# Kernel tuning notes

Measured on AMD Instinct MI355X. Metric: run time of the kernel, lower is better.

## Reference

```python
import jax, jax.numpy as jnp
import numpy as np
from jax import lax

K = 3      # kernel_size
PAD = 1    # padding
OG = 2     # offset groups


def _conv2d(x, w, b):
    y = lax.conv_general_dilated(x, w, (1, 1), [(PAD, PAD), (PAD, PAD)],
                                 dimension_numbers=('NCHW', 'OIHW', 'NCHW'))
    return y + b[None, :, None, None]


def _deform_conv2d(x, offset, mask, weight):
    # torchvision-style modulated deform_conv2d (v2), stride=1, dilation=1,
    # zero out-of-bounds, offset layout [B, OG*K*K*2, H, W] with (dy, dx) pairs.
    B, C, H, W = x.shape
    O = weight.shape[0]
    K2 = K * K
    Cg = C // OG

    ki, kj = jnp.meshgrid(jnp.arange(K), jnp.arange(K), indexing='ij')
    ki = ki.reshape(K2)
    kj = kj.reshape(K2)
    base_y = jnp.arange(H)[None, :] - PAD + ki[:, None]   # [K2, H]
    base_x = jnp.arange(W)[None, :] - PAD + kj[:, None]   # [K2, W]

    off = offset.reshape(B, OG, K2, 2, H, W)
    py = off[:, :, :, 0] + base_y[None, None, :, :, None].astype(x.dtype)  # [B,OG,K2,H,W]
    px = off[:, :, :, 1] + base_x[None, None, :, None, :].astype(x.dtype)
    m = mask.reshape(B, OG, K2, H, W)

    y0f = jnp.floor(py)
    x0f = jnp.floor(px)
    wy1 = py - y0f   # bilinear weights, grads flow through py/px
    wx1 = px - x0f
    y0 = y0f.astype(jnp.int32)
    x0 = x0f.astype(jnp.int32)
    y1 = y0 + 1
    x1 = x0 + 1

    img = x.reshape(B, OG, Cg, H * W)

    def gather(yi, xi):
        valid = (yi >= 0) & (yi < H) & (xi >= 0) & (xi < W)
        idx = jnp.clip(yi, 0, H - 1) * W + jnp.clip(xi, 0, W - 1)          # [B,OG,K2,H,W]
        v = jnp.take_along_axis(img[:, :, :, None, :],
                                idx.reshape(B, OG, 1, K2, H * W), axis=-1)
        return v.reshape(B, OG, Cg, K2, H, W) * valid[:, :, None].astype(x.dtype)

    v00 = gather(y0, x0)
    v01 = gather(y0, x1)
    v10 = gather(y1, x0)
    v11 = gather(y1, x1)

    wy1e = wy1[:, :, None]   # [B,OG,1,K2,H,W]
    wx1e = wx1[:, :, None]
    val = (v00 * (1 - wy1e) * (1 - wx1e)
           + v01 * (1 - wy1e) * wx1e
           + v10 * wy1e * (1 - wx1e)
           + v11 * wy1e * wx1e)
    val = val * m[:, :, None]                               # modulation mask

    wr = weight.reshape(O, OG, Cg, K2)
    return jnp.einsum('ogck,bgckhw->bohw', wr, val)


def setup_inputs() -> dict:
    key = jax.random.key(0)
    k1, k2, k3, k4, k5 = jax.random.split(key, 5)
    B, C, O, H, W = 4, 64, 64, 128, 128
    K2 = K * K
    x = jax.random.normal(k1, (B, C, H, W), dtype=jnp.float32)
    w_main = jax.random.normal(k2, (O, C, K, K), dtype=jnp.float32) / np.sqrt(C * K2)
    w_off = jax.random.normal(k3, (2 * OG * K2, C, K, K), dtype=jnp.float32) * 0.01
    b_off = jax.random.normal(k4, (2 * OG * K2,), dtype=jnp.float32) * 0.01
    w_mask = jnp.full((OG * K2, C, K, K), 0.5, dtype=jnp.float32)  # init_mask = 0.5
    b_mask = jax.random.normal(k5, (OG * K2,), dtype=jnp.float32) * 0.01
    return {"x": x, "w_main": w_main, "w_off": w_off, "b_off": b_off,
            "w_mask": w_mask, "b_mask": b_mask}


def reference(x, w_main, w_off, b_off, w_mask, b_mask):
    offset = _conv2d(x, w_off, b_off)
    mask = jax.nn.sigmoid(_conv2d(x, w_mask, b_mask))
    return _deform_conv2d(x, offset, mask, w_main)
```

## Files before the change

kernel.cpp:

```cpp
#include <hip/hip_runtime.h>
#include <math.h>

#define BB 4
#define C 64
#define O 64
#define H 128
#define W 128
#define OG 2
#define Cg 32
#define K2 9
#define HW (H*W)
#define NOFF 36
#define NMSK 18

typedef __bf16 bf16;
typedef bf16 bf16x8 __attribute__((ext_vector_type(8)));
typedef float f32x4 __attribute__((ext_vector_type(4)));
typedef unsigned short u16x4 __attribute__((ext_vector_type(4)));

#define VSTR 288
#define BSTR 60

__device__ inline unsigned short f2h_bits(float f) {
  _Float16 h = (_Float16)f;
  return __builtin_bit_cast(unsigned short, h);
}
__device__ inline float h2f(unsigned short u) {
  return (float)__builtin_bit_cast(_Float16, u);
}

__global__ __launch_bounds__(256) void transpose_nhwc(
    const float* __restrict__ x, unsigned short* __restrict__ xT) {
  __shared__ float tile[64][65];
  int tid = threadIdx.x;
  int b = blockIdx.x >> 8;
  int p0 = (blockIdx.x & 255) * 64;
#pragma unroll
  for (int it = 0; it < 16; ++it) {
    int c = it * 4 + (tid >> 6);
    tile[c][tid & 63] = x[((size_t)(b * C + c)) * HW + p0 + (tid & 63)];
  }
  __syncthreads();
#pragma unroll
  for (int it = 0; it < 4; ++it) {
    int p = it * 16 + (tid >> 4);
    int cg = tid & 15;
    u16x4 o;
#pragma unroll
    for (int j = 0; j < 4; ++j) {
      bf16 t = (bf16)tile[cg * 4 + j][p];
      o[j] = __builtin_bit_cast(unsigned short, t);
    }
    *(u16x4*)&xT[((size_t)(b * HW + p0 + p)) * C + cg * 4] = o;
  }
}

__global__ __launch_bounds__(256) void prep_w(
    const float* __restrict__ w_main, const float* __restrict__ w_off,
    const float* __restrict__ w_mask, bf16* __restrict__ wfC,
    bf16* __restrict__ wfM) {
  int i = blockIdx.x * 256 + threadIdx.x;
  int which = (i >= 36864);
  int ii = which ? i - 36864 : i;
  int j = ii & 7;
  int l = (ii >> 3) & 63;
  int rest = ii >> 9;
  int to = rest & 3;
  int kk = (rest >> 2) % 9;
  int ph = (rest >> 2) / 9;
  int m = to * 16 + (l & 15);
  int u = kk * 32 + (l >> 4) * 8 + j;
  int tap = u >> 5;
  int c1 = u & 31;
  float v;
  if (!which) {
    int c = ph * 32 + c1;
    v = (m < NOFF) ? w_off[(m * C + c) * K2 + tap]
        : (m < 54) ? w_mask[((m - NOFF) * C + c) * K2 + tap]
                   : 0.f;
    wfC[ii] = (bf16)v;
  } else {
    v = w_main[(m * C + ph * 32 + c1) * K2 + tap];
    wfM[ii] = (bf16)v;
  }
}

__global__ __launch_bounds__(256, 3) void fused_deform(
    const bf16* __restrict__ xT, const bf16* __restrict__ wfC,
    const bf16* __restrict__ wfM, const float* __restrict__ b_off,
    const float* __restrict__ b_mask, float* __restrict__ out) {
  __shared__ bf16 val[64][VSTR];
  __shared__ unsigned int buf[64][BSTR];
  float* bufF = (float*)&buf[0][0];

  const int tid = threadIdx.x;
  const int lane = tid & 63;
  const int wv = tid >> 6;
  const int n16 = lane & 15;
  const int q4 = lane >> 4;
  const int chunk = tid & 3;
  const int pg = tid >> 2;

  const int b = blockIdx.x >> 8;
  const int ti = blockIdx.x & 255;
  const int h0 = ti >> 1;
  const int w0 = (ti & 1) * 64;
  const bf16* xb = xT + (size_t)b * HW * C;

  bf16x8 zero8;
#pragma unroll
  for (int j = 0; j < 8; ++j) zero8[j] = (bf16)0.f;

  f32x4 accC[4] = {{0.f,0.f,0.f,0.f},{0.f,0.f,0.f,0.f},
                   {0.f,0.f,0.f,0.f},{0.f,0.f,0.f,0.f}};
#pragma unroll 1
  for (int ph = 0; ph < 2; ++ph) {
    if (ph) __syncthreads();
#pragma unroll
    for (int tap = 0; tap < 9; ++tap) {
      int yy = h0 + tap / 3 - 1;
      int xx = w0 + pg + tap % 3 - 1;
      bf16x8 v = zero8;
      if ((unsigned)yy < (unsigned)H) {
        int xc = min(max(xx, 0), W - 1);
        bf16x8 t = *(const bf16x8*)(xb + (size_t)((yy << 7) + xc) * C + ph * 32 + chunk * 8);
        if ((unsigned)xx < (unsigned)W) v = t;
      }
      *(bf16x8*)&val[pg][tap * 32 + chunk * 8] = v;
    }
    __syncthreads();
    const bf16* wb = wfC + (size_t)ph * (9 * 4 * 64 * 8);
#pragma unroll
    for (int kk = 0; kk < 9; ++kk) {
      bf16x8 bfr = *(const bf16x8*)&val[wv * 16 + n16][kk * 32 + q4 * 8];
#pragma unroll
      for (int to = 0; to < 4; ++to) {
        bf16x8 afr = *(const bf16x8*)(wb + (size_t)((kk * 4 + to) * 64 + lane) * 8);
        accC[to] = __builtin_amdgcn_mfma_f32_16x16x32_bf16(afr, bfr, accC[to], 0, 0, 0);
      }
    }
  }
  {
    int p = wv * 16 + n16;
#pragma unroll
    for (int to = 0; to < 4; ++to)
#pragma unroll
      for (int r = 0; r < 4; ++r) {
        int o = to * 16 + q4 * 4 + r;
        float a = accC[to][r];
        if (o < NOFF) {
          bufF[p * BSTR + o] = a + b_off[o];
        } else if (o < 54) {
          float s = a + b_mask[o - NOFF];
          bufF[p * BSTR + o] = 1.f / (1.f + __expf(-s));
        }
      }
  }
  __syncthreads();

  unsigned int rW0[5], rW1[5], rCo[5];
#pragma unroll
  for (int it = 0; it < 5; ++it) {
    int t = it * 256 + tid;
    if (t < 1152) {
      int p = t & 63;
      int gk = t >> 6;
      int g = gk / 9, tap = gk % 9;
      float offy = bufF[p * BSTR + 2 * gk];
      float offx = bufF[p * BSTR + 2 * gk + 1];
      float m = bufF[p * BSTR + NOFF + gk];
      float py = offy + (float)(h0 + tap / 3 - 1);
      float px = offx + (float)(w0 + p + tap % 3 - 1);
      float y0f = floorf(py), x0f = floorf(px);
      float wy1 = py - y0f, wx1 = px - x0f;
      float wy0 = 1.f - wy1, wx0 = 1.f - wx1;
      int y0 = (int)y0f, x0 = (int)x0f;
      int y1 = y0 + 1, x1 = x0 + 1;
      bool y0ok = (unsigned)y0 < (unsigned)H, y1ok = (unsigned)y1 < (unsigned)H;
      bool x0ok = (unsigned)x0 < (unsigned)W, x1ok = (unsigned)x1 < (unsigned)W;
      float w00 = (y0ok && x0ok) ? wy0 * wx0 * m : 0.f;
      float w01 = (y0ok && x1ok) ? wy0 * wx1 * m : 0.f;
      float w10 = (y1ok && x0ok) ? wy1 * wx0 * m : 0.f;
      float w11 = (y1ok && x1ok) ? wy1 * wx1 * m : 0.f;
      unsigned int y0c = (unsigned)min(max(y0, 0), H - 1);
      unsigned int y1c = (unsigned)min(max(y1, 0), H - 1);
      unsigned int x0c = (unsigned)min(max(x0, 0), W - 1);
      unsigned int x1c = (unsigned)min(max(x1, 0), W - 1);
      rW0[it] = (unsigned)f2h_bits(w00) | ((unsigned)f2h_bits(w01) << 16);
      rW1[it] = (unsigned)f2h_bits(w10) | ((unsigned)f2h_bits(w11) << 16);
      rCo[it] = y0c | (x0c << 8) | (y1c << 16) | (x1c << 24);
    }
  }
  __syncthreads();
#pragma unroll
  for (int it = 0; it < 5; ++it) {
    int t = it * 256 + tid;
    if (t < 1152) {
      int p = t & 63;
      int gk = t >> 6;
      buf[p][2 * gk] = rW0[it];
      buf[p][2 * gk + 1] = rW1[it];
      buf[p][NOFF + gk] = rCo[it];
    }
  }
  __syncthreads();

  f32x4 accM[4] = {{0.f,0.f,0.f,0.f},{0.f,0.f,0.f,0.f},
                   {0.f,0.f,0.f,0.f},{0.f,0.f,0.f,0.f}};
#pragma unroll 1
  for (int g = 0; g < 2; ++g) {
    if (g) __syncthreads();
    const bf16* bb = xb + g * 32 + chunk * 8;
#pragma unroll 3
    for (int tap = 0; tap < 9; ++tap) {
      int gk = g * 9 + tap;
      unsigned int wab = buf[pg][2 * gk];
      unsigned int wcd = buf[pg][2 * gk + 1];
      unsigned int pk = buf[pg][NOFF + gk];
      float w00 = h2f(wab & 0xffff), w01 = h2f(wab >> 16);
      float w10 = h2f(wcd & 0xffff), w11 = h2f(wcd >> 16);
      int r0 = (int)(pk & 255) << 7;
      int x0 = (int)((pk >> 8) & 255);
      int r1 = (int)((pk >> 16) & 255) << 7;
      int x1 = (int)(pk >> 24);
      bf16x8 v00 = *(const bf16x8*)(bb + (size_t)(r0 + x0) * C);
      bf16x8 v01 = *(const bf16x8*)(bb + (size_t)(r0 + x1) * C);
      bf16x8 v10 = *(const bf16x8*)(bb + (size_t)(r1 + x0) * C);
      bf16x8 v11 = *(const bf16x8*)(bb + (size_t)(r1 + x1) * C);
      bf16x8 res;
#pragma unroll
      for (int j = 0; j < 8; ++j) {
        float v = (float)v00[j] * w00 + (float)v01[j] * w01 +
                  (float)v10[j] * w10 + (float)v11[j] * w11;
        res[j] = (bf16)v;
      }
      *(bf16x8*)&val[pg][tap * 32 + chunk * 8] = res;
    }
    __syncthreads();
    const bf16* wb = wfM + (size_t)g * (9 * 4 * 64 * 8);
#pragma unroll
    for (int kk = 0; kk < 9; ++kk) {
      bf16x8 bfr = *(const bf16x8*)&val[wv * 16 + n16][kk * 32 + q4 * 8];
#pragma unroll
      for (int to = 0; to < 4; ++to) {
        bf16x8 afr = *(const bf16x8*)(wb + (size_t)((kk * 4 + to) * 64 + lane) * 8);
        accM[to] = __builtin_amdgcn_mfma_f32_16x16x32_bf16(afr, bfr, accM[to], 0, 0, 0);
      }
    }
  }

  {
    int p = wv * 16 + n16;
    float* ob = out + (size_t)b * O * HW + (h0 << 7) + w0 + p;
#pragma unroll
    for (int to = 0; to < 4; ++to)
#pragma unroll
      for (int r = 0; r < 4; ++r) {
        int o = to * 16 + q4 * 4 + r;
        ob[(size_t)o * HW] = accM[to][r];
      }
  }
}

extern "C" void kernel_launch(void* const* d_in, const int* in_sizes, int n_in,
                              void* d_out, int out_size, void* d_ws,
                              size_t ws_size, hipStream_t stream) {
  const float* x = (const float*)d_in[0];
  const float* w_main = (const float*)d_in[1];
  const float* w_off = (const float*)d_in[2];
  const float* b_off = (const float*)d_in[3];
  const float* w_mask = (const float*)d_in[4];
  const float* b_mask = (const float*)d_in[5];
  float* out = (float*)d_out;

  bf16* xT = (bf16*)d_ws;
  bf16* wfC = xT + (size_t)BB * HW * C;
  bf16* wfM = wfC + 36864;

  transpose_nhwc<<<1024, 256, 0, stream>>>(x, (unsigned short*)xT);
  prep_w<<<288, 256, 0, stream>>>(w_main, w_off, w_mask, wfC, wfM);
  fused_deform<<<1024, 256, 0, stream>>>(xT, wfC, wfM, b_off, b_mask, out);
}
```

Baseline: 130.6 us.

## Stage conv halo once, prefetch second half, coalesce output stores, merge prep kernels

```diff
diff --git a/kernel.cpp b/kernel.cpp
--- a/kernel.cpp
+++ b/kernel.cpp
@@ -6,8 +6,6 @@
 #define O 64
 #define H 128
 #define W 128
-#define OG 2
-#define Cg 32
 #define K2 9
 #define HW (H*W)
 #define NOFF 36
@@ -20,6 +18,8 @@
 
 #define VSTR 288
 #define BSTR 60
+#define VAL_BYTES 36864
+#define NW_TOTAL 73728
 
 __device__ inline unsigned short f2h_bits(float f) {
   _Float16 h = (_Float16)f;
@@ -29,8 +29,11 @@
   return (float)__builtin_bit_cast(_Float16, u);
 }
 
-__global__ __launch_bounds__(256) void transpose_nhwc(
-    const float* __restrict__ x, unsigned short* __restrict__ xT) {
+__global__ __launch_bounds__(256) void prep_all(
+    const float* __restrict__ x, const float* __restrict__ w_main,
+    const float* __restrict__ w_off, const float* __restrict__ w_mask,
+    unsigned short* __restrict__ xT16, bf16* __restrict__ wfC,
+    bf16* __restrict__ wfM) {
   __shared__ float tile[64][65];
   int tid = threadIdx.x;
   int b = blockIdx.x >> 8;
@@ -38,50 +41,58 @@
 #pragma unroll
   for (int it = 0; it < 16; ++it) {
     int c = it * 4 + (tid >> 6);
-    tile[c][tid & 63] = x[((size_t)(b * C + c)) * HW + p0 + (tid & 63)];
+    tile[c][tid & 63] = x[(size_t)(b * C + c) * HW + p0 + (tid & 63)];
   }
   __syncthreads();
 #pragma unroll
   for (int it = 0; it < 4; ++it) {
     int p = it * 16 + (tid >> 4);
-    int cg = tid & 15;
+    int cq = tid & 15;
     u16x4 o;
 #pragma unroll
     for (int j = 0; j < 4; ++j) {
-      bf16 t = (bf16)tile[cg * 4 + j][p];
+      bf16 t = (bf16)tile[cq * 4 + j][p];
       o[j] = __builtin_bit_cast(unsigned short, t);
     }
-    *(u16x4*)&xT[((size_t)(b * HW + p0 + p)) * C + cg * 4] = o;
-  }
-}
-
-__global__ __launch_bounds__(256) void prep_w(
-    const float* __restrict__ w_main, const float* __restrict__ w_off,
-    const float* __restrict__ w_mask, bf16* __restrict__ wfC,
-    bf16* __restrict__ wfM) {
-  int i = blockIdx.x * 256 + threadIdx.x;
-  int which = (i >= 36864);
-  int ii = which ? i - 36864 : i;
-  int j = ii & 7;
-  int l = (ii >> 3) & 63;
-  int rest = ii >> 9;
-  int to = rest & 3;
-  int kk = (rest >> 2) % 9;
-  int ph = (rest >> 2) / 9;
-  int m = to * 16 + (l & 15);
-  int u = kk * 32 + (l >> 4) * 8 + j;
-  int tap = u >> 5;
-  int c1 = u & 31;
-  float v;
-  if (!which) {
-    int c = ph * 32 + c1;
-    v = (m < NOFF) ? w_off[(m * C + c) * K2 + tap]
-        : (m < 54) ? w_mask[((m - NOFF) * C + c) * K2 + tap]
-                   : 0.f;
-    wfC[ii] = (bf16)v;
-  } else {
-    v = w_main[(m * C + ph * 32 + c1) * K2 + tap];
-    wfM[ii] = (bf16)v;
+    *(u16x4*)&xT16[(size_t)(b * HW + p0 + p) * C + cq * 4] = o;
+  }
+  int i = blockIdx.x * 256 + tid;
+  if (i < NW_TOTAL) {
+    int which = (i >= 36864);
+    int ii = which ? i - 36864 : i;
+    int j = ii & 7;
+    int l = (ii >> 3) & 63;
+    int rest = ii >> 9;
+    int to = rest & 3;
+    int kk = (rest >> 2) % 9;
+    int ph = (rest >> 2) / 9;
+    int m = to * 16 + (l & 15);
+    int u = kk * 32 + (l >> 4) * 8 + j;
+    int tap = u >> 5;
+    int c1 = u & 31;
+    if (!which) {
+      int c = ph * 32 + c1;
+      float v = (m < NOFF) ? w_off[(m * C + c) * K2 + tap]
+                : (m < 54) ? w_mask[((m - NOFF) * C + c) * K2 + tap]
+                           : 0.f;
+      wfC[ii] = (bf16)v;
+    } else {
+      wfM[ii] = (bf16)w_main[(m * C + ph * 32 + c1) * K2 + tap];
+    }
+  }
+}
+
+__device__ inline void mfma9(const bf16* __restrict__ wb,
+                             const bf16 (*val)[VSTR], int row, int q4,
+                             int lane, f32x4* acc) {
+#pragma unroll
+  for (int kk = 0; kk < 9; ++kk) {
+    bf16x8 bfr = *(const bf16x8*)&val[row][kk * 32 + q4 * 8];
+#pragma unroll
+    for (int to = 0; to < 4; ++to) {
+      bf16x8 afr = *(const bf16x8*)(wb + (size_t)((kk * 4 + to) * 64 + lane) * 8);
+      acc[to] = __builtin_amdgcn_mfma_f32_16x16x32_bf16(afr, bfr, acc[to], 0, 0, 0);
+    }
   }
 }
 
@@ -89,9 +100,12 @@
     const bf16* __restrict__ xT, const bf16* __restrict__ wfC,
     const bf16* __restrict__ wfM, const float* __restrict__ b_off,
     const float* __restrict__ b_mask, float* __restrict__ out) {
-  __shared__ bf16 val[64][VSTR];
-  __shared__ unsigned int buf[64][BSTR];
-  float* bufF = (float*)&buf[0][0];
+  __shared__ __align__(16) char smem[52224];
+  bf16 (*val)[VSTR] = (bf16 (*)[VSTR])smem;
+  unsigned int (*buf)[BSTR] = (unsigned int (*)[BSTR])(smem + VAL_BYTES);
+  float* bufF = (float*)(smem + VAL_BYTES);
+  bf16x8* stage16 = (bf16x8*)(smem + VAL_BYTES);
+  float* valF = (float*)smem;
 
   const int tid = threadIdx.x;
   const int lane = tid & 63;
@@ -113,33 +127,60 @@
 
   f32x4 accC[4] = {{0.f,0.f,0.f,0.f},{0.f,0.f,0.f,0.f},
                    {0.f,0.f,0.f,0.f},{0.f,0.f,0.f,0.f}};
-#pragma unroll 1
-  for (int ph = 0; ph < 2; ++ph) {
-    if (ph) __syncthreads();
-#pragma unroll
-    for (int tap = 0; tap < 9; ++tap) {
-      int yy = h0 + tap / 3 - 1;
-      int xx = w0 + pg + tap % 3 - 1;
+#pragma unroll
+  for (int it = 0; it < 4; ++it) {
+    int id = it * 256 + tid;
+    if (id < 816) {
+      int q2 = id & 3;
+      int wp = (id >> 2) % 68;
+      int r = (id >> 2) / 68;
+      int yy = h0 + r - 1;
+      int xx = w0 + wp - 1;
       bf16x8 v = zero8;
-      if ((unsigned)yy < (unsigned)H) {
-        int xc = min(max(xx, 0), W - 1);
-        bf16x8 t = *(const bf16x8*)(xb + (size_t)((yy << 7) + xc) * C + ph * 32 + chunk * 8);
-        if ((unsigned)xx < (unsigned)W) v = t;
-      }
-      *(bf16x8*)&val[pg][tap * 32 + chunk * 8] = v;
-    }
-    __syncthreads();
-    const bf16* wb = wfC + (size_t)ph * (9 * 4 * 64 * 8);
-#pragma unroll
-    for (int kk = 0; kk < 9; ++kk) {
-      bf16x8 bfr = *(const bf16x8*)&val[wv * 16 + n16][kk * 32 + q4 * 8];
-#pragma unroll
-      for (int to = 0; to < 4; ++to) {
-        bf16x8 afr = *(const bf16x8*)(wb + (size_t)((kk * 4 + to) * 64 + lane) * 8);
-        accC[to] = __builtin_amdgcn_mfma_f32_16x16x32_bf16(afr, bfr, accC[to], 0, 0, 0);
-      }
-    }
-  }
+      if ((unsigned)yy < (unsigned)H && (unsigned)xx < (unsigned)W)
+        v = *(const bf16x8*)(xb + (size_t)((yy << 7) + xx) * C + q2 * 8);
+      stage16[id] = v;
+    }
+  }
+  __syncthreads();
+#pragma unroll
+  for (int tap = 0; tap < 9; ++tap) {
+    bf16x8 v = stage16[((tap / 3) * 68 + pg + tap % 3) * 4 + chunk];
+    *(bf16x8*)&val[pg][tap * 32 + chunk * 8] = v;
+  }
+  __syncthreads();
+  bf16x8 pre[4];
+  int preid[4];
+#pragma unroll
+  for (int it = 0; it < 4; ++it) {
+    int id = it * 256 + tid;
+    preid[it] = (id < 816) ? id : -1;
+    bf16x8 v = zero8;
+    if (id < 816) {
+      int q2 = id & 3;
+      int wp = (id >> 2) % 68;
+      int r = (id >> 2) / 68;
+      int yy = h0 + r - 1;
+      int xx = w0 + wp - 1;
+      if ((unsigned)yy < (unsigned)H && (unsigned)xx < (unsigned)W)
+        v = *(const bf16x8*)(xb + (size_t)((yy << 7) + xx) * C + 32 + q2 * 8);
+    }
+    pre[it] = v;
+  }
+  mfma9(wfC, val, wv * 16 + n16, q4, lane, accC);
+  __syncthreads();
+#pragma unroll
+  for (int it = 0; it < 4; ++it)
+    if (preid[it] >= 0) stage16[preid[it]] = pre[it];
+  __syncthreads();
+#pragma unroll
+  for (int tap = 0; tap < 9; ++tap) {
+    bf16x8 v = stage16[((tap / 3) * 68 + pg + tap % 3) * 4 + chunk];
+    *(bf16x8*)&val[pg][tap * 32 + chunk * 8] = v;
+  }
+  __syncthreads();
+  mfma9(wfC + 9 * 4 * 64 * 8, val, wv * 16 + n16, q4, lane, accC);
+
   {
     int p = wv * 16 + n16;
 #pragma unroll
@@ -237,28 +278,28 @@
       *(bf16x8*)&val[pg][tap * 32 + chunk * 8] = res;
     }
     __syncthreads();
-    const bf16* wb = wfM + (size_t)g * (9 * 4 * 64 * 8);
-#pragma unroll
-    for (int kk = 0; kk < 9; ++kk) {
-      bf16x8 bfr = *(const bf16x8*)&val[wv * 16 + n16][kk * 32 + q4 * 8];
-#pragma unroll
-      for (int to = 0; to < 4; ++to) {
-        bf16x8 afr = *(const bf16x8*)(wb + (size_t)((kk * 4 + to) * 64 + lane) * 8);
-        accM[to] = __builtin_amdgcn_mfma_f32_16x16x32_bf16(afr, bfr, accM[to], 0, 0, 0);
-      }
-    }
-  }
-
+    mfma9(wfM + (size_t)g * (9 * 4 * 64 * 8), val, wv * 16 + n16, q4, lane, accM);
+  }
+
+  __syncthreads();
   {
     int p = wv * 16 + n16;
-    float* ob = out + (size_t)b * O * HW + (h0 << 7) + w0 + p;
 #pragma unroll
     for (int to = 0; to < 4; ++to)
 #pragma unroll
-      for (int r = 0; r < 4; ++r) {
-        int o = to * 16 + q4 * 4 + r;
-        ob[(size_t)o * HW] = accM[to][r];
-      }
+      for (int r = 0; r < 4; ++r)
+        valF[(to * 16 + q4 * 4 + r) * 68 + p] = accM[to][r];
+  }
+  __syncthreads();
+  {
+    float* ob = out + (size_t)b * O * HW + (h0 << 7) + w0;
+#pragma unroll
+    for (int it = 0; it < 4; ++it) {
+      int id = it * 256 + tid;
+      int o = id >> 4, seg = id & 15;
+      f32x4 v = *(f32x4*)&valF[o * 68 + seg * 4];
+      *(f32x4*)&ob[(size_t)o * HW + seg * 4] = v;
+    }
   }
 }
 
@@ -273,11 +314,11 @@
   const float* b_mask = (const float*)d_in[5];
   float* out = (float*)d_out;
 
-  bf16* xT = (bf16*)d_ws;
-  bf16* wfC = xT + (size_t)BB * HW * C;
+  unsigned short* xT16 = (unsigned short*)d_ws;
+  bf16* wfC = (bf16*)(xT16 + (size_t)BB * HW * C);
   bf16* wfM = wfC + 36864;
 
-  transpose_nhwc<<<1024, 256, 0, stream>>>(x, (unsigned short*)xT);
-  prep_w<<<288, 256, 0, stream>>>(w_main, w_off, w_mask, wfC, wfM);
-  fused_deform<<<1024, 256, 0, stream>>>(xT, wfC, wfM, b_off, b_mask, out);
-}
+  prep_all<<<1024, 256, 0, stream>>>(x, w_main, w_off, w_mask, xT16, wfC, wfM);
+  fused_deform<<<1024, 256, 0, stream>>>((const bf16*)xT16, wfC, wfM, b_off,
+                                         b_mask, out);
+}
```

Result: slower. 147.7 us (+13.1%).
